# Kernel tuning notes

Measured on AMD Instinct MI355X. Metric: run time of the kernel, lower is better.

The kernel has to match this reference:

```python
import jax, jax.numpy as jnp
import numpy as np

A = 32          # num input capsule types
PSIZE = 16      # caps_size (pose matrix 4x4)
MD = 4          # mat_dim = sqrt(caps_size)
NCLS = 10       # output capsules / classes
KF = 5          # routing kernel (final_shape)
KK = KF * KF
KKA = KK * A
ITERS = 3
FINAL_LAMBDA = 0.01
EPS = 1e-12
LN2PI = float(np.log(2.0 * np.pi))
BN_EPS = 1e-5


def unfold(x, k, stride, pad):
    # torch.nn.functional.unfold: [b,C,h,w] -> [b, C*k*k, L], (c, kh, kw) channel-major
    b, c, h, w = x.shape
    if pad:
        x = jnp.pad(x, ((0, 0), (0, 0), (pad, pad), (pad, pad)))
    oh = (h + 2 * pad - k) // stride + 1
    ow = (w + 2 * pad - k) // stride + 1
    cols = jnp.stack([
        jnp.stack([x[:, :, i:i + stride * oh:stride, j:j + stride * ow:stride]
                   for j in range(k)], axis=3)
        for i in range(k)], axis=2)          # [b, c, k, k, oh, ow]
    return cols.reshape(b, c * k * k, oh * ow)


def conv3x3(x, w):
    return jax.lax.conv_general_dilated(x, w, (1, 1), [(1, 1), (1, 1)],
                                        dimension_numbers=('NCHW', 'OIHW', 'NCHW'))


def bn_inf(x, g, b, m, v):
    scale = g / jnp.sqrt(v + BN_EPS)
    return (x - m[None, :, None, None]) * scale[None, :, None, None] + b[None, :, None, None]


def em_routing(a_in, pose, W, beta_u, beta_a):
    b = a_in.shape[0]
    # pose votes
    pu = unfold(pose, KF, 1, 0)                     # [b, A*PSIZE*KK, l]
    l = pu.shape[-1]
    pu = pu.reshape(b, A, PSIZE, KK, l).transpose(0, 4, 3, 1, 2).reshape(b, l, KKA, PSIZE)
    pm = pu.reshape(b, l, KKA, MD, MD)[:, :, :, None]        # [b,l,kkA,1,md,md]
    v = jnp.matmul(pm, W)                                    # [b,l,kkA,B,md,md]
    v = v.reshape(b, l, KKA, NCLS, PSIZE)
    # activations
    au = unfold(a_in, KF, 1, 0).reshape(b, A, KK, l).transpose(0, 3, 2, 1).reshape(b, l, KKA)
    r = jnp.ones((b, l, KKA, NCLS, 1), v.dtype)
    a_out = mu = None
    for i in range(ITERS):
        lam = FINAL_LAMBDA * (1.0 - 0.95 ** (i + 1))
        # M-step
        rw = r * au[:, :, :, None, None]
        r_sum = rw.sum(axis=2, keepdims=True)                # [b,l,1,B,1]
        coeff = rw / (r_sum + EPS)
        mu = (coeff * v).sum(axis=2, keepdims=True)          # [b,l,1,B,psize]
        sigma_sq = (coeff * (v - mu) ** 2).sum(axis=2, keepdims=True) + EPS
        r_s = r_sum[:, :, 0]                                 # [b,l,B,1]
        sig = sigma_sq[:, :, 0]                              # [b,l,B,psize]
        cost_h = (beta_u + 0.5 * jnp.log(sig)) * r_s         # log(sqrt(s)) = 0.5*log(s)
        a_out = jax.nn.sigmoid(lam * (beta_a - cost_h.sum(axis=3)))   # [b,l,B]
        if i < ITERS - 1:
            # E-step (note: log(sigma_sq * ln2pi) as in original code)
            ln_p = (-0.5 * jnp.sum(jnp.log(sigma_sq * LN2PI), axis=-1)
                    - jnp.sum((v - mu) ** 2 / (2.0 * sigma_sq), axis=-1))   # [b,l,kkA,B]
            ln_ap = ln_p + jnp.log(a_out)[:, :, None, :]
            r = jax.nn.softmax(ln_ap, axis=-1)[..., None]
    oh = int(np.floor(np.sqrt(l)))
    pose_out = mu[:, :, 0].reshape(b, l, -1).transpose(0, 2, 1).reshape(b, -1, oh, oh)
    a_map = a_out.transpose(0, 2, 1).reshape(b, -1, oh, oh)
    return a_map, pose_out


def setup_inputs():
    key = jax.random.key(0)
    ks = jax.random.split(key, 14)
    batch = 256
    x = jax.random.normal(ks[0], (batch, 512, 5, 5), jnp.float32)
    w_a = jax.random.normal(ks[1], (A, 512, 3, 3), jnp.float32) * 0.02
    w_pose = jax.random.normal(ks[2], (A * PSIZE, 512, 3, 3), jnp.float32) * 0.02
    bn_a_g = 1.0 + 0.1 * jax.random.normal(ks[3], (A,), jnp.float32)
    bn_a_b = 0.1 * jax.random.normal(ks[4], (A,), jnp.float32)
    bn_a_m = 0.1 * jax.random.normal(ks[5], (A,), jnp.float32)
    bn_a_v = jax.random.uniform(ks[6], (A,), jnp.float32, 0.5, 1.5)
    C2 = A * PSIZE
    bn_p_g = 1.0 + 0.1 * jax.random.normal(ks[7], (C2,), jnp.float32)
    bn_p_b = 0.1 * jax.random.normal(ks[8], (C2,), jnp.float32)
    bn_p_m = 0.1 * jax.random.normal(ks[9], (C2,), jnp.float32)
    bn_p_v = jax.random.uniform(ks[10], (C2,), jnp.float32, 0.5, 1.5)
    W = jax.random.normal(ks[11], (KKA, NCLS, MD, MD), jnp.float32) * 0.25
    beta_u = jnp.zeros((1, 1, NCLS, 1), jnp.float32)
    beta_a = jnp.zeros((1, 1, NCLS), jnp.float32)
    return {"x": x, "w_a": w_a, "w_pose": w_pose,
            "bn_a_g": bn_a_g, "bn_a_b": bn_a_b, "bn_a_m": bn_a_m, "bn_a_v": bn_a_v,
            "bn_p_g": bn_p_g, "bn_p_b": bn_p_b, "bn_p_m": bn_p_m, "bn_p_v": bn_p_v,
            "W": W, "beta_u": beta_u, "beta_a": beta_a}


def reference(x, w_a, w_pose, bn_a_g, bn_a_b, bn_a_m, bn_a_v,
              bn_p_g, bn_p_b, bn_p_m, bn_p_v, W, beta_u, beta_a):
    a = jax.nn.sigmoid(bn_inf(conv3x3(x, w_a), bn_a_g, bn_a_b, bn_a_m, bn_a_v))
    pose = bn_inf(conv3x3(x, w_pose), bn_p_g, bn_p_b, bn_p_m, bn_p_v)
    a_map, _ = em_routing(a, pose, W, beta_u, beta_a)
    out = a_map.reshape(a_map.shape[0], -1)          # [b, 10]
    out = out / out.sum(axis=1, keepdims=True)
    return jnp.log(out)
```

## Files before the change

kernel.cpp:

```cpp
#include <hip/hip_runtime.h>
#include <math.h>

#define CIN 512
#define NCLS 10
#define KDIM 4608
#define NTOT 6400
#define MPAD 640
#define BK 128
#define NKT 36
#define NABLK (5 * NKT)
#define LN2PI_F 1.8378770664093453f

typedef __attribute__((ext_vector_type(8))) short bf16x8;
typedef __attribute__((ext_vector_type(4))) float f32x4;

typedef const __attribute__((address_space(1))) void* gas_ptr;
typedef __attribute__((address_space(3))) void* las_ptr;

__device__ __forceinline__ void async_copy16(const void* g, void* l) {
    __builtin_amdgcn_global_load_lds((gas_ptr)g, (las_ptr)l, 16, 0, 0);
}

__device__ __forceinline__ unsigned short f2bf(float f) {
    unsigned int u = __float_as_uint(f);
    u = (u + 0x7fffu + ((u >> 16) & 1u)) >> 16;
    return (unsigned short)u;
}
__device__ __forceinline__ float bf2f(unsigned short s) {
    return __uint_as_float(((unsigned int)s) << 16);
}
__device__ __forceinline__ float fexp(float x) { return __expf(x); }
__device__ __forceinline__ float flog(float x) { return __logf(x); }

__global__ __launch_bounds__(256) void pack_a_kernel(
    const float* __restrict__ w_pose, const float* __restrict__ w_a,
    const float* __restrict__ bn_p_g, const float* __restrict__ bn_p_b,
    const float* __restrict__ bn_p_m, const float* __restrict__ bn_p_v,
    const float* __restrict__ bn_a_g, const float* __restrict__ bn_a_b,
    const float* __restrict__ bn_a_m, const float* __restrict__ bn_a_v,
    const float* __restrict__ Wm,
    unsigned short* __restrict__ At, unsigned short* __restrict__ Wmb,
    float* __restrict__ sc, float* __restrict__ bi)
{
    const int blk = blockIdx.x;
    const int t = threadIdx.x;

    if (blk >= NABLK) {
        const int chunk = (blk - NABLK) * 256 + t;
        if (chunk < 16000) {
            const int e = chunk >> 1, half = chunk & 1;
            const int m = e / 10, c = e - m * 10;
            const int kk = m >> 5, a = m & 31;
            const int de = (kk * 10 + c) * 32 + a;
            const float4* s4 = reinterpret_cast<const float4*>(Wm + (size_t)chunk * 8);
            float4 x0 = s4[0], x1 = s4[1];
            int4 o;
            o.x = (int)f2bf(x0.x) | ((int)f2bf(x0.y) << 16);
            o.y = (int)f2bf(x0.z) | ((int)f2bf(x0.w) << 16);
            o.z = (int)f2bf(x1.x) | ((int)f2bf(x1.y) << 16);
            o.w = (int)f2bf(x1.z) | ((int)f2bf(x1.w) << 16);
            reinterpret_cast<int4*>(Wmb + ((size_t)de * 2 + half) * 8)[0] = o;
        }
        return;
    }

    const int mblk = blk / NKT;
    if (blk == 0) {
        for (int i = t; i < MPAD; i += 256) {
            float s = 0.f, b = 0.f;
            if (i < 512) {
                s = bn_p_g[i] / sqrtf(bn_p_v[i] + 1e-5f);
                b = bn_p_b[i] - bn_p_m[i] * s;
            } else if (i < 544) {
                const int j = i - 512;
                s = bn_a_g[j] / sqrtf(bn_a_v[j] + 1e-5f);
                b = bn_a_b[j] - bn_a_m[j] * s;
            }
            sc[i] = s; bi[i] = b;
        }
    }

    const int kt = blk - mblk * NKT;
    #pragma unroll
    for (int j = 0; j < 8; ++j) {
        const int c = t + j * 256;
        const int kc8 = c >> 7, slot = c & 127;
        const int row = mblk * 128 + (slot ^ (kc8 << 2));
        const int k0 = (kt * 16 + kc8) * 8;
        float v[8] = {0.f,0.f,0.f,0.f,0.f,0.f,0.f,0.f};
        if (row < 512) {
            const float4* s4 = reinterpret_cast<const float4*>(w_pose + (size_t)row * KDIM + k0);
            float4 x0 = s4[0], x1 = s4[1];
            v[0]=x0.x; v[1]=x0.y; v[2]=x0.z; v[3]=x0.w;
            v[4]=x1.x; v[5]=x1.y; v[6]=x1.z; v[7]=x1.w;
        } else if (row < 544) {
            const float4* s4 = reinterpret_cast<const float4*>(w_a + (size_t)(row - 512) * KDIM + k0);
            float4 x0 = s4[0], x1 = s4[1];
            v[0]=x0.x; v[1]=x0.y; v[2]=x0.z; v[3]=x0.w;
            v[4]=x1.x; v[5]=x1.y; v[6]=x1.z; v[7]=x1.w;
        }
        int4 o;
        o.x = (int)f2bf(v[0]) | ((int)f2bf(v[1]) << 16);
        o.y = (int)f2bf(v[2]) | ((int)f2bf(v[3]) << 16);
        o.z = (int)f2bf(v[4]) | ((int)f2bf(v[5]) << 16);
        o.w = (int)f2bf(v[6]) | ((int)f2bf(v[7]) << 16);
        reinterpret_cast<int4*>(At + ((((size_t)blk) << 11) + c) * 8)[0] = o;
    }
}

__global__ __launch_bounds__(1024) void pack_b_kernel(
    const float* __restrict__ x, unsigned short* __restrict__ Bt)
{
    __shared__ __align__(16) float xs[CIN * 25];
    const int b = blockIdx.x;
    const int t = threadIdx.x;
    const float4* xb = reinterpret_cast<const float4*>(x + (size_t)b * (CIN * 25));
    for (int f4 = t; f4 < (CIN * 25) / 4; f4 += 1024)
        reinterpret_cast<float4*>(xs)[f4] = xb[f4];
    __syncthreads();

    for (int w = t; w < 25 * (KDIM / 8); w += 1024) {
        const int ch = w / 25;
        const int px = w - ch * 25;
        const int py = px / 5, qx = px % 5;
        const int k0 = ch * 8;
        unsigned short v[8];
        #pragma unroll
        for (int j = 0; j < 8; ++j) {
            const int k = k0 + j;
            const int ci = k / 9;
            const int kk = k - ci * 9;
            const int dy = kk / 3, dx = kk - dy * 3;
            const int yy = py + dy - 1, xx = qx + dx - 1;
            const bool ok = (yy >= 0) & (yy < 5) & (xx >= 0) & (xx < 5);
            v[j] = ok ? f2bf(xs[ci * 25 + yy * 5 + xx]) : (unsigned short)0;
        }
        int4 o;
        o.x = (int)v[0] | ((int)v[1] << 16);
        o.y = (int)v[2] | ((int)v[3] << 16);
        o.z = (int)v[4] | ((int)v[5] << 16);
        o.w = (int)v[6] | ((int)v[7] << 16);
        const int n = b * 25 + px;
        const int nblk = n >> 7, nr = n & 127;
        const int kt = k0 >> 7;
        const int kc8 = (k0 >> 3) & 15;
        const int c = kc8 * 128 + (nr ^ (kc8 << 2));
        reinterpret_cast<int4*>(Bt + ((((size_t)(nblk * NKT + kt)) << 11) + c) * 8)[0] = o;
    }
}

__global__ __launch_bounds__(1024) void gemm_kernel(
    const unsigned short* __restrict__ At,
    const unsigned short* __restrict__ Bt,
    const float* __restrict__ sc, const float* __restrict__ bi,
    unsigned short* __restrict__ Cp,
    float* __restrict__ Ca)
{
    __shared__ __align__(16) unsigned char smem[131072];
    const int t = threadIdx.x;
    const int L = blockIdx.x;
    int mblk, nblk;
    if (L >= 240) { const int i = L - 240; mblk = i >> 1; nblk = 48 + (i & 1); }
    else          { const int q = L / 40, r = L - q * 40;
                    mblk = r >> 3; nblk = q * 8 + (r & 7); }
    const int m0 = mblk * 128, n0 = nblk * 128;
    const int lane = t & 63, w = t >> 6;
    const int g = w >> 2, wq = w & 3;
    const int wm = wq >> 1, wn = wq & 1;
    const int row16 = lane & 15, quad = lane >> 4;

    f32x4 acc[4][4] = {};

    const unsigned short* gAbase = At + (((size_t)mblk * NKT) << 14);
    const unsigned short* gBbase = Bt + (((size_t)nblk * NKT) << 14);

    #define STAGE(kt, s)                                                      \
    {                                                                         \
        unsigned short* As_ = (unsigned short*)(smem + (s) * 65536);          \
        unsigned short* Bs_ = As_ + 16384;                                    \
        const unsigned short* ga = gAbase + ((size_t)(kt) << 14);             \
        const unsigned short* gb = gBbase + ((size_t)(kt) << 14);             \
        _Pragma("unroll")                                                     \
        for (int j = 0; j < 2; ++j) {                                         \
            async_copy16(ga + ((size_t)(j * 1024 + t) << 3),                  \
                         As_ + ((size_t)(j * 1024 + w * 64) << 3));           \
            async_copy16(gb + ((size_t)(j * 1024 + t) << 3),                  \
                         Bs_ + ((size_t)(j * 1024 + w * 64) << 3));           \
        }                                                                     \
    }

    #define COMPUTE(s)                                                        \
    {                                                                         \
        const unsigned short* As_ = (const unsigned short*)(smem + (s) * 65536);\
        const unsigned short* Bs_ = As_ + 16384;                              \
        const int kc8b = g * 4 + quad;                                        \
        const int sw = kc8b << 2;                                             \
        bf16x8 af[4], bfr[4];                                                 \
        _Pragma("unroll")                                                     \
        for (int mt = 0; mt < 4; ++mt)                                        \
            af[mt] = *reinterpret_cast<const bf16x8*>(                        \
                &As_[(size_t)(kc8b * 128 + ((wm * 64 + mt * 16 + row16) ^ sw)) * 8]);\
        _Pragma("unroll")                                                     \
        for (int nt = 0; nt < 4; ++nt)                                        \
            bfr[nt] = *reinterpret_cast<const bf16x8*>(                       \
                &Bs_[(size_t)(kc8b * 128 + ((wn * 64 + nt * 16 + row16) ^ sw)) * 8]);\
        _Pragma("unroll")                                                     \
        for (int mt = 0; mt < 4; ++mt)                                        \
            _Pragma("unroll")                                                 \
            for (int nt = 0; nt < 4; ++nt)                                    \
                acc[mt][nt] = __builtin_amdgcn_mfma_f32_16x16x32_bf16(        \
                    af[mt], bfr[nt], acc[mt][nt], 0, 0, 0);                   \
    }

    STAGE(0, 0);
    for (int kt = 0; kt < NKT; ++kt) {
        __syncthreads();
        if (kt + 1 < NKT) STAGE(kt + 1, (kt + 1) & 1);
        COMPUTE(kt & 1);
    }
    #undef STAGE
    #undef COMPUTE

    f32x4* mb = (f32x4*)smem;
    #pragma unroll
    for (int r = 1; r < 4; ++r) {
        __syncthreads();
        if (g == r) {
            f32x4* dst = mb + wq * 1024;
            #pragma unroll
            for (int i = 0; i < 16; ++i)
                dst[i * 64 + lane] = acc[i >> 2][i & 3];
        }
        __syncthreads();
        if (g == 0) {
            const f32x4* src = mb + wq * 1024;
            #pragma unroll
            for (int i = 0; i < 16; ++i)
                acc[i >> 2][i & 3] += src[i * 64 + lane];
        }
    }

    if (g == 0) {
        #pragma unroll
        for (int mt = 0; mt < 4; ++mt) {
            const int mbase = m0 + wm * 64 + mt * 16 + quad * 4;
            if (mbase >= 544) continue;
            #pragma unroll
            for (int rg = 0; rg < 4; ++rg) {
                const int m = mbase + rg;
                const float s = sc[m], bbx = bi[m];
                #pragma unroll
                for (int nt = 0; nt < 4; ++nt) {
                    const int n = n0 + wn * 64 + nt * 16 + row16;
                    const float v = fmaf(acc[mt][nt][rg], s, bbx);
                    if (m < 512) Cp[(size_t)m * NTOT + n] = f2bf(v);
                    else Ca[(size_t)(m - 512) * NTOT + n] = 1.f / (1.f + fexp(-v));
                }
            }
        }
    }
}

__global__ __launch_bounds__(640, 1) void em_kernel(
    const unsigned short* __restrict__ Cp,
    const float* __restrict__ Ca,
    const unsigned short* __restrict__ Wmb,
    const float* __restrict__ beta_u, const float* __restrict__ beta_a,
    float* __restrict__ out)
{
    __shared__ __align__(16) unsigned short psh[25][2][32][8];
    __shared__ float aush[800];
    __shared__ float lnq[NCLS][800];
    __shared__ float mu_sh[NCLS][16];
    __shared__ float i2s_sh[NCLS][16];
    __shared__ float costp[2][NCLS];
    __shared__ float slgp[2][NCLS];
    __shared__ float Kc_sh[NCLS];
    __shared__ float aout_sh[NCLS];

    const int b = blockIdx.x, t = threadIdx.x;
    const int c = t >> 6;
    const int rh = (t >> 5) & 1;
    const int a = t & 31;

    const unsigned short* pb = Cp + (size_t)b * 25;
    for (int f = t; f < 12800; f += 640) {
        const int c2 = f / 25, px = f - c2 * 25;
        const int e = c2 & 15;
        psh[px][e >> 3][c2 >> 4][e & 7] = pb[(size_t)c2 * NTOT + px];
    }
    const float* ab = Ca + (size_t)b * 25;
    for (int f = t; f < 800; f += 640) {
        const int ci = f / 25, px = f - ci * 25;
        aush[px * 32 + ci] = ab[(size_t)ci * NTOT + px];
    }
    __syncthreads();

    const float bu = beta_u[c], ba = beta_a[c];
    float muL[8], i2sL[8], KcL = 0.f;
    const unsigned short* wbase = Wmb + ((size_t)(c * 32 + a)) * 16;

    #define VOTE(w0_, w1_, p_, vv)                                           \
        {                                                                    \
            float pm[8], wv[16];                                             \
            const unsigned int pu[4] = {(unsigned)p_.x, (unsigned)p_.y,      \
                                        (unsigned)p_.z, (unsigned)p_.w};     \
            _Pragma("unroll")                                                \
            for (int i = 0; i < 4; ++i) {                                    \
                pm[2*i]   = __uint_as_float(pu[i] << 16);                    \
                pm[2*i+1] = __uint_as_float(pu[i] & 0xFFFF0000u);            \
            }                                                                \
            const unsigned int uu[8] = {(unsigned)w0_.x,(unsigned)w0_.y,     \
                (unsigned)w0_.z,(unsigned)w0_.w,(unsigned)w1_.x,             \
                (unsigned)w1_.y,(unsigned)w1_.z,(unsigned)w1_.w};            \
            _Pragma("unroll")                                                \
            for (int i = 0; i < 8; ++i) {                                    \
                wv[2*i]   = __uint_as_float(uu[i] << 16);                    \
                wv[2*i+1] = __uint_as_float(uu[i] & 0xFFFF0000u);            \
            }                                                                \
            _Pragma("unroll")                                                \
            for (int jr = 0; jr < 2; ++jr) {                                 \
                _Pragma("unroll")                                            \
                for (int s = 0; s < 4; ++s) {                                \
                    float av = 0.f;                                          \
                    _Pragma("unroll")                                        \
                    for (int tt = 0; tt < 4; ++tt)                           \
                        av = fmaf(pm[jr*4+tt], wv[tt*4+s], av);              \
                    vv[jr*4+s] = av;                                         \
                }                                                            \
            }                                                                \
        }

    float p95 = 1.f;
    for (int it = 0; it < 3; ++it) {
        p95 *= 0.95f;
        const float lam = 0.01f * (1.f - p95);

        if (it > 0) {
            int4 wr0 = *reinterpret_cast<const int4*>(wbase);
            int4 wr1 = *reinterpret_cast<const int4*>(wbase + 8);
            int4 pr  = *reinterpret_cast<const int4*>(&psh[0][rh][a][0]);
            for (int kk = 0; kk < 25; ++kk) {
                const int4 w0 = wr0, w1 = wr1, p = pr;
                if (kk < 24) {
                    const unsigned short* wn = wbase + (size_t)(kk + 1) * 5120;
                    wr0 = *reinterpret_cast<const int4*>(wn);
                    wr1 = *reinterpret_cast<const int4*>(wn + 8);
                    pr  = *reinterpret_cast<const int4*>(&psh[kk + 1][rh][a][0]);
                }
                float vv[8];
                VOTE(w0, w1, p, vv);
                float q = (rh == 0) ? KcL : 0.f;
                #pragma unroll
                for (int j = 0; j < 8; ++j) {
                    const float d = vv[j] - muL[j];
                    q -= d * d * i2sL[j];
                }
                q += __shfl_xor(q, 32);
                if (rh == 0) lnq[c][kk * 32 + a] = q;
            }
            __syncthreads();
            for (int m = t; m < 800; m += 640) {
                float qv[NCLS];
                #pragma unroll
                for (int cc = 0; cc < NCLS; ++cc) qv[cc] = lnq[cc][m];
                float mx = qv[0];
                #pragma unroll
                for (int cc = 1; cc < NCLS; ++cc) mx = fmaxf(mx, qv[cc]);
                float ev[NCLS];
                float den = 0.f;
                #pragma unroll
                for (int cc = 0; cc < NCLS; ++cc) {
                    ev[cc] = fexp(qv[cc] - mx);
                    den += ev[cc];
                }
                const float s = aush[m] * __builtin_amdgcn_rcpf(den);
                #pragma unroll
                for (int cc = 0; cc < NCLS; ++cc)
                    lnq[cc][m] = ev[cc] * s;
            }
            __syncthreads();
        }

        float S0 = 0.f, S1[8], S2[8];
        #pragma unroll
        for (int j = 0; j < 8; ++j) { S1[j] = 0.f; S2[j] = 0.f; }

        int4 wA0 = *reinterpret_cast<const int4*>(wbase);
        int4 wA1 = *reinterpret_cast<const int4*>(wbase + 8);
        int4 wB0 = *reinterpret_cast<const int4*>(wbase + 5120);
        int4 wB1 = *reinterpret_cast<const int4*>(wbase + 5120 + 8);
        int4 pr  = *reinterpret_cast<const int4*>(&psh[0][rh][a][0]);
        for (int kk = 0; kk < 25; ++kk) {
            const int4 w0 = wA0, w1 = wA1, p = pr;
            wA0 = wB0; wA1 = wB1;
            if (kk < 23) {
                const unsigned short* wn = wbase + (size_t)(kk + 2) * 5120;
                wB0 = *reinterpret_cast<const int4*>(wn);
                wB1 = *reinterpret_cast<const int4*>(wn + 8);
            }
            if (kk < 24)
                pr = *reinterpret_cast<const int4*>(&psh[kk + 1][rh][a][0]);
            float vv[8];
            VOTE(w0, w1, p, vv);
            const int m = kk * 32 + a;
            const float rw = (it == 0) ? aush[m] : lnq[c][m];
            S0 += rw;
            #pragma unroll
            for (int j = 0; j < 8; ++j) {
                const float rv = rw * vv[j];
                S1[j] += rv;
                S2[j] = fmaf(rv, vv[j], S2[j]);
            }
        }

        #pragma unroll
        for (int off = 16; off >= 1; off >>= 1) {
            S0 += __shfl_xor(S0, off);
            #pragma unroll
            for (int j = 0; j < 8; ++j) {
                S1[j] += __shfl_xor(S1[j], off);
                S2[j] += __shfl_xor(S2[j], off);
            }
        }

        if (a == 0) {
            const float s0e = S0 + 1e-12f;
            const float inv = 1.f / s0e;
            float cost_ = 0.f, slg_ = 0.f;
            #pragma unroll
            for (int j = 0; j < 8; ++j) {
                const float mu_ = S1[j] * inv;
                const float sg = (S2[j] - 2.f * mu_ * S1[j] + mu_ * mu_ * S0) * inv
                                 + 1e-12f;
                cost_ += bu + 0.5f * flog(sg);
                slg_ += flog(sg * LN2PI_F);
                mu_sh[c][rh * 8 + j] = mu_;
                i2s_sh[c][rh * 8 + j] = 0.5f / sg;
            }
            costp[rh][c] = cost_;
            slgp[rh][c] = slg_;
        }
        __syncthreads();
        if (a == 0 && rh == 0) {
            const float costsum = (costp[0][c] + costp[1][c]) * S0;
            const float aout = 1.f / (1.f + fexp(-(lam * (ba - costsum))));
            aout_sh[c] = aout;
            Kc_sh[c] = flog(aout) - 0.5f * (slgp[0][c] + slgp[1][c]);
        }
        __syncthreads();
        if (it < 2) {
            #pragma unroll
            for (int j = 0; j < 8; ++j) {
                muL[j] = mu_sh[c][rh * 8 + j];
                i2sL[j] = i2s_sh[c][rh * 8 + j];
            }
            KcL = Kc_sh[c];
        }
    }

    if (t < NCLS) {
        float s = 0.f;
        #pragma unroll
        for (int cc = 0; cc < NCLS; ++cc) s += aout_sh[cc];
        out[b * NCLS + t] = flog(aout_sh[t] / s);
    }
    #undef VOTE
}

extern "C" void kernel_launch(void* const* d_in, const int* in_sizes, int n_in,
                              void* d_out, int out_size, void* d_ws, size_t ws_size,
                              hipStream_t stream) {
    const float* x      = (const float*)d_in[0];
    const float* w_a    = (const float*)d_in[1];
    const float* w_pose = (const float*)d_in[2];
    const float* bn_a_g = (const float*)d_in[3];
    const float* bn_a_b = (const float*)d_in[4];
    const float* bn_a_m = (const float*)d_in[5];
    const float* bn_a_v = (const float*)d_in[6];
    const float* bn_p_g = (const float*)d_in[7];
    const float* bn_p_b = (const float*)d_in[8];
    const float* bn_p_m = (const float*)d_in[9];
    const float* bn_p_v = (const float*)d_in[10];
    const float* Wm     = (const float*)d_in[11];
    const float* beta_u = (const float*)d_in[12];
    const float* beta_a = (const float*)d_in[13];
    float* out = (float*)d_out;

    char* p = (char*)d_ws;
    unsigned short* At  = (unsigned short*)p;  p += (size_t)MPAD * KDIM * 2;
    unsigned short* Bt  = (unsigned short*)p;  p += (size_t)NTOT * KDIM * 2;
    unsigned short* Wmb = (unsigned short*)p;  p += (size_t)800 * NCLS * 16 * 2;
    unsigned short* Cp  = (unsigned short*)p;  p += (size_t)512 * NTOT * 2;
    float* Ca = (float*)p;                     p += (size_t)32 * NTOT * 4;
    float* sc = (float*)p;                     p += MPAD * 4;
    float* bi = (float*)p;                     p += MPAD * 4;

    pack_a_kernel<<<NABLK + 63, 256, 0, stream>>>(w_pose, w_a,
                                                  bn_p_g, bn_p_b, bn_p_m, bn_p_v,
                                                  bn_a_g, bn_a_b, bn_a_m, bn_a_v,
                                                  Wm, At, Wmb, sc, bi);
    pack_b_kernel<<<256, 1024, 0, stream>>>(x, Bt);
    gemm_kernel<<<250, 1024, 0, stream>>>(At, Bt, sc, bi, Cp, Ca);
    em_kernel<<<256, 640, 0, stream>>>(Cp, Ca, Wmb, beta_u, beta_a, out);
}
```

Measured before the change: 227.0 us.

## Merge pack kernels and stage EM routing weights through LDS with async copies

Combines the A/W packing kernel and the im2col B packing kernel into one launch, removing a kernel boundary. In the EM kernel, the per-thread global loads of the transformation matrices are replaced by double-buffered async global-to-LDS copies in chunks of four kernel positions, read back with a swizzled index. This aims to cut launch overhead and make weight loads coalesced and overlapped with compute. In exchange it adds about 80KB of LDS and a block barrier per chunk in every routing pass, and the merged pack kernel's 1024-thread blocks reserve 51KB of LDS even where it is unused.

```diff
diff --git a/kernel.cpp b/kernel.cpp
--- a/kernel.cpp
+++ b/kernel.cpp
@@ -32,7 +32,8 @@
 __device__ __forceinline__ float fexp(float x) { return __expf(x); }
 __device__ __forceinline__ float flog(float x) { return __logf(x); }
 
-__global__ __launch_bounds__(256) void pack_a_kernel(
+__global__ __launch_bounds__(1024) void pack_kernel(
+    const float* __restrict__ x,
     const float* __restrict__ w_pose, const float* __restrict__ w_a,
     const float* __restrict__ bn_p_g, const float* __restrict__ bn_p_b,
     const float* __restrict__ bn_p_m, const float* __restrict__ bn_p_v,
@@ -40,13 +41,57 @@
     const float* __restrict__ bn_a_m, const float* __restrict__ bn_a_v,
     const float* __restrict__ Wm,
     unsigned short* __restrict__ At, unsigned short* __restrict__ Wmb,
-    float* __restrict__ sc, float* __restrict__ bi)
+    float* __restrict__ sc, float* __restrict__ bi,
+    unsigned short* __restrict__ Bt)
 {
-    const int blk = blockIdx.x;
+    __shared__ __align__(16) float xs[CIN * 25];
+    const int bid = blockIdx.x;
     const int t = threadIdx.x;
 
-    if (blk >= NABLK) {
-        const int chunk = (blk - NABLK) * 256 + t;
+    if (bid < 256) {
+        const int b = bid;
+        const float4* xb = reinterpret_cast<const float4*>(x + (size_t)b * (CIN * 25));
+        for (int f4 = t; f4 < (CIN * 25) / 4; f4 += 1024)
+            reinterpret_cast<float4*>(xs)[f4] = xb[f4];
+        __syncthreads();
+
+        for (int w = t; w < 25 * (KDIM / 8); w += 1024) {
+            const int ch = w / 25;
+            const int px = w - ch * 25;
+            const int py = px / 5, qx = px % 5;
+            const int k0 = ch * 8;
+            unsigned short v[8];
+            #pragma unroll
+            for (int j = 0; j < 8; ++j) {
+                const int k = k0 + j;
+                const int ci = k / 9;
+                const int kk = k - ci * 9;
+                const int dy = kk / 3, dx = kk - dy * 3;
+                const int yy = py + dy - 1, xx = qx + dx - 1;
+                const bool ok = (yy >= 0) & (yy < 5) & (xx >= 0) & (xx < 5);
+                v[j] = ok ? f2bf(xs[ci * 25 + yy * 5 + xx]) : (unsigned short)0;
+            }
+            int4 o;
+            o.x = (int)v[0] | ((int)v[1] << 16);
+            o.y = (int)v[2] | ((int)v[3] << 16);
+            o.z = (int)v[4] | ((int)v[5] << 16);
+            o.w = (int)v[6] | ((int)v[7] << 16);
+            const int n = b * 25 + px;
+            const int nblk = n >> 7, nr = n & 127;
+            const int kt = k0 >> 7;
+            const int kc8 = (k0 >> 3) & 15;
+            const int c = kc8 * 128 + (nr ^ (kc8 << 2));
+            reinterpret_cast<int4*>(Bt + ((((size_t)(nblk * NKT + kt)) << 11) + c) * 8)[0] = o;
+        }
+        return;
+    }
+
+    const int f = (bid - 256) * 1024 + t;
+    const int vblk = f >> 8, vt = f & 255;
+    if (vblk >= NABLK + 63) return;
+
+    if (vblk >= NABLK) {
+        const int chunk = (vblk - NABLK) * 256 + vt;
         if (chunk < 16000) {
             const int e = chunk >> 1, half = chunk & 1;
             const int m = e / 10, c = e - m * 10;
@@ -64,9 +109,9 @@
         return;
     }
 
-    const int mblk = blk / NKT;
-    if (blk == 0) {
-        for (int i = t; i < MPAD; i += 256) {
+    const int mblk = vblk / NKT;
+    if (vblk == 0) {
+        for (int i = vt; i < MPAD; i += 256) {
             float s = 0.f, b = 0.f;
             if (i < 512) {
                 s = bn_p_g[i] / sqrtf(bn_p_v[i] + 1e-5f);
@@ -80,10 +125,10 @@
         }
     }
 
-    const int kt = blk - mblk * NKT;
+    const int kt = vblk - mblk * NKT;
     #pragma unroll
     for (int j = 0; j < 8; ++j) {
-        const int c = t + j * 256;
+        const int c = vt + j * 256;
         const int kc8 = c >> 7, slot = c & 127;
         const int row = mblk * 128 + (slot ^ (kc8 << 2));
         const int k0 = (kt * 16 + kc8) * 8;
@@ -104,48 +149,7 @@
         o.y = (int)f2bf(v[2]) | ((int)f2bf(v[3]) << 16);
         o.z = (int)f2bf(v[4]) | ((int)f2bf(v[5]) << 16);
         o.w = (int)f2bf(v[6]) | ((int)f2bf(v[7]) << 16);
-        reinterpret_cast<int4*>(At + ((((size_t)blk) << 11) + c) * 8)[0] = o;
-    }
-}
-
-__global__ __launch_bounds__(1024) void pack_b_kernel(
-    const float* __restrict__ x, unsigned short* __restrict__ Bt)
-{
-    __shared__ __align__(16) float xs[CIN * 25];
-    const int b = blockIdx.x;
-    const int t = threadIdx.x;
-    const float4* xb = reinterpret_cast<const float4*>(x + (size_t)b * (CIN * 25));
-    for (int f4 = t; f4 < (CIN * 25) / 4; f4 += 1024)
-        reinterpret_cast<float4*>(xs)[f4] = xb[f4];
-    __syncthreads();
-
-    for (int w = t; w < 25 * (KDIM / 8); w += 1024) {
-        const int ch = w / 25;
-        const int px = w - ch * 25;
-        const int py = px / 5, qx = px % 5;
-        const int k0 = ch * 8;
-        unsigned short v[8];
-        #pragma unroll
-        for (int j = 0; j < 8; ++j) {
-            const int k = k0 + j;
-            const int ci = k / 9;
-            const int kk = k - ci * 9;
-            const int dy = kk / 3, dx = kk - dy * 3;
-            const int yy = py + dy - 1, xx = qx + dx - 1;
-            const bool ok = (yy >= 0) & (yy < 5) & (xx >= 0) & (xx < 5);
-            v[j] = ok ? f2bf(xs[ci * 25 + yy * 5 + xx]) : (unsigned short)0;
-        }
-        int4 o;
-        o.x = (int)v[0] | ((int)v[1] << 16);
-        o.y = (int)v[2] | ((int)v[3] << 16);
-        o.z = (int)v[4] | ((int)v[5] << 16);
-        o.w = (int)v[6] | ((int)v[7] << 16);
-        const int n = b * 25 + px;
-        const int nblk = n >> 7, nr = n & 127;
-        const int kt = k0 >> 7;
-        const int kc8 = (k0 >> 3) & 15;
-        const int c = kc8 * 128 + (nr ^ (kc8 << 2));
-        reinterpret_cast<int4*>(Bt + ((((size_t)(nblk * NKT + kt)) << 11) + c) * 8)[0] = o;
+        reinterpret_cast<int4*>(At + ((((size_t)vblk) << 11) + c) * 8)[0] = o;
     }
 }
 
@@ -269,6 +273,7 @@
     float* __restrict__ out)
 {
     __shared__ __align__(16) unsigned short psh[25][2][32][8];
+    __shared__ __align__(16) unsigned short wsh[2 * 20480];
     __shared__ float aush[800];
     __shared__ float lnq[NCLS][800];
     __shared__ float mu_sh[NCLS][16];
@@ -283,6 +288,20 @@
     const int rh = (t >> 5) & 1;
     const int a = t & 31;
 
+    const int gu = t ^ ((t >> 3) & 3);
+    const int r2 = (c * 32 + a) * 2;
+    const int u0 = r2 ^ ((r2 >> 3) & 3);
+
+    #define STAGEW(qq, ss)                                                   \
+    {                                                                        \
+        const int nkk_ = ((qq) == 6) ? 1 : 4;                                \
+        const unsigned short* gW = Wmb + (size_t)(qq) * 4 * 5120;            \
+        unsigned short* lW = wsh + (size_t)(ss) * 20480;                     \
+        for (int kki = 0; kki < nkk_; ++kki)                                 \
+            async_copy16(gW + (size_t)(kki * 640 + gu) * 8,                  \
+                         lW + (size_t)(kki * 640 + t) * 8);                  \
+    }
+
     const unsigned short* pb = Cp + (size_t)b * 25;
     for (int f = t; f < 12800; f += 640) {
         const int c2 = f / 25, px = f - c2 * 25;
@@ -298,7 +317,6 @@
 
     const float bu = beta_u[c], ba = beta_a[c];
     float muL[8], i2sL[8], KcL = 0.f;
-    const unsigned short* wbase = Wmb + ((size_t)(c * 32 + a)) * 16;
 
     #define VOTE(w0_, w1_, p_, vv)                                           \
         {                                                                    \
@@ -337,29 +355,33 @@
         const float lam = 0.01f * (1.f - p95);
 
         if (it > 0) {
-            int4 wr0 = *reinterpret_cast<const int4*>(wbase);
-            int4 wr1 = *reinterpret_cast<const int4*>(wbase + 8);
-            int4 pr  = *reinterpret_cast<const int4*>(&psh[0][rh][a][0]);
-            for (int kk = 0; kk < 25; ++kk) {
-                const int4 w0 = wr0, w1 = wr1, p = pr;
-                if (kk < 24) {
-                    const unsigned short* wn = wbase + (size_t)(kk + 1) * 5120;
-                    wr0 = *reinterpret_cast<const int4*>(wn);
-                    wr1 = *reinterpret_cast<const int4*>(wn + 8);
-                    pr  = *reinterpret_cast<const int4*>(&psh[kk + 1][rh][a][0]);
+            STAGEW(0, 0);
+            __syncthreads();
+            for (int qc = 0; qc < 7; ++qc) {
+                if (qc < 6) STAGEW(qc + 1, (qc + 1) & 1);
+                const unsigned short* wb = wsh + (size_t)(qc & 1) * 20480;
+                #pragma unroll
+                for (int kkin = 0; kkin < 4; ++kkin) {
+                    const int kk = qc * 4 + kkin;
+                    if (kk < 25) {
+                        const unsigned short* wrow = wb + kkin * 5120;
+                        const int4 w0 = *reinterpret_cast<const int4*>(wrow + (size_t)u0 * 8);
+                        const int4 w1 = *reinterpret_cast<const int4*>(wrow + (size_t)(u0 ^ 1) * 8);
+                        const int4 p = *reinterpret_cast<const int4*>(&psh[kk][rh][a][0]);
+                        float vv[8];
+                        VOTE(w0, w1, p, vv);
+                        float qacc = (rh == 0) ? KcL : 0.f;
+                        #pragma unroll
+                        for (int j = 0; j < 8; ++j) {
+                            const float d = vv[j] - muL[j];
+                            qacc -= d * d * i2sL[j];
+                        }
+                        qacc += __shfl_xor(qacc, 32);
+                        if (rh == 0) lnq[c][kk * 32 + a] = qacc;
+                    }
                 }
-                float vv[8];
-                VOTE(w0, w1, p, vv);
-                float q = (rh == 0) ? KcL : 0.f;
-                #pragma unroll
-                for (int j = 0; j < 8; ++j) {
-                    const float d = vv[j] - muL[j];
-                    q -= d * d * i2sL[j];
-                }
-                q += __shfl_xor(q, 32);
-                if (rh == 0) lnq[c][kk * 32 + a] = q;
-            }
-            __syncthreads();
+                __syncthreads();
+            }
             for (int m = t; m < 800; m += 640) {
                 float qv[NCLS];
                 #pragma unroll
@@ -386,32 +408,33 @@
         #pragma unroll
         for (int j = 0; j < 8; ++j) { S1[j] = 0.f; S2[j] = 0.f; }
 
-        int4 wA0 = *reinterpret_cast<const int4*>(wbase);
-        int4 wA1 = *reinterpret_cast<const int4*>(wbase + 8);
-        int4 wB0 = *reinterpret_cast<const int4*>(wbase + 5120);
-        int4 wB1 = *reinterpret_cast<const int4*>(wbase + 5120 + 8);
-        int4 pr  = *reinterpret_cast<const int4*>(&psh[0][rh][a][0]);
-        for (int kk = 0; kk < 25; ++kk) {
-            const int4 w0 = wA0, w1 = wA1, p = pr;
-            wA0 = wB0; wA1 = wB1;
-            if (kk < 23) {
-                const unsigned short* wn = wbase + (size_t)(kk + 2) * 5120;
-                wB0 = *reinterpret_cast<const int4*>(wn);
-                wB1 = *reinterpret_cast<const int4*>(wn + 8);
-            }
-            if (kk < 24)
-                pr = *reinterpret_cast<const int4*>(&psh[kk + 1][rh][a][0]);
-            float vv[8];
-            VOTE(w0, w1, p, vv);
-            const int m = kk * 32 + a;
-            const float rw = (it == 0) ? aush[m] : lnq[c][m];
-            S0 += rw;
-            #pragma unroll
-            for (int j = 0; j < 8; ++j) {
-                const float rv = rw * vv[j];
-                S1[j] += rv;
-                S2[j] = fmaf(rv, vv[j], S2[j]);
-            }
+        STAGEW(0, 0);
+        __syncthreads();
+        for (int qc = 0; qc < 7; ++qc) {
+            if (qc < 6) STAGEW(qc + 1, (qc + 1) & 1);
+            const unsigned short* wb = wsh + (size_t)(qc & 1) * 20480;
+            #pragma unroll
+            for (int kkin = 0; kkin < 4; ++kkin) {
+                const int kk = qc * 4 + kkin;
+                if (kk < 25) {
+                    const unsigned short* wrow = wb + kkin * 5120;
+                    const int4 w0 = *reinterpret_cast<const int4*>(wrow + (size_t)u0 * 8);
+                    const int4 w1 = *reinterpret_cast<const int4*>(wrow + (size_t)(u0 ^ 1) * 8);
+                    const int4 p = *reinterpret_cast<const int4*>(&psh[kk][rh][a][0]);
+                    float vv[8];
+                    VOTE(w0, w1, p, vv);
+                    const int m = kk * 32 + a;
+                    const float rw = (it == 0) ? aush[m] : lnq[c][m];
+                    S0 += rw;
+                    #pragma unroll
+                    for (int j = 0; j < 8; ++j) {
+                        const float rv = rw * vv[j];
+                        S1[j] += rv;
+                        S2[j] = fmaf(rv, vv[j], S2[j]);
+                    }
+                }
+            }
+            __syncthreads();
         }
 
         #pragma unroll
@@ -466,6 +489,7 @@
         out[b * NCLS + t] = flog(aout_sh[t] / s);
     }
     #undef VOTE
+    #undef STAGEW
 }
 
 extern "C" void kernel_launch(void* const* d_in, const int* in_sizes, int n_in,
@@ -496,11 +520,10 @@
     float* sc = (float*)p;                     p += MPAD * 4;
     float* bi = (float*)p;                     p += MPAD * 4;
 
-    pack_a_kernel<<<NABLK + 63, 256, 0, stream>>>(w_pose, w_a,
-                                                  bn_p_g, bn_p_b, bn_p_m, bn_p_v,
-                                                  bn_a_g, bn_a_b, bn_a_m, bn_a_v,
-                                                  Wm, At, Wmb, sc, bi);
-    pack_b_kernel<<<256, 1024, 0, stream>>>(x, Bt);
+    pack_kernel<<<317, 1024, 0, stream>>>(x, w_pose, w_a,
+                                          bn_p_g, bn_p_b, bn_p_m, bn_p_v,
+                                          bn_a_g, bn_a_b, bn_a_m, bn_a_v,
+                                          Wm, At, Wmb, sc, bi, Bt);
     gemm_kernel<<<250, 1024, 0, stream>>>(At, Bt, sc, bi, Cp, Ca);
     em_kernel<<<256, 640, 0, stream>>>(Cp, Ca, Wmb, beta_u, beta_a, out);
 }
```

Result: no change. 230.9 us (+1.7%).

## Split EM routing per batch across two workgroups with flag-synchronized partial sums

Applied to the files above, without the earlier changes.

Each batch element's EM routing is now handled by two blocks, each processing about half of the 25 kernel positions, doubling the grid to 512 blocks. After each M-step reduction, the blocks publish their partial sums to global memory and exchange them via release/acquire flags before continuing. This aims to use more CUs and shorten the serial per-block loop. The cost is extra global traffic, spin-wait synchronization, and a reliance on paired blocks being co-resident to avoid deadlock.

```diff
diff --git a/kernel.cpp b/kernel.cpp
--- a/kernel.cpp
+++ b/kernel.cpp
@@ -40,7 +40,8 @@
     const float* __restrict__ bn_a_m, const float* __restrict__ bn_a_v,
     const float* __restrict__ Wm,
     unsigned short* __restrict__ At, unsigned short* __restrict__ Wmb,
-    float* __restrict__ sc, float* __restrict__ bi)
+    float* __restrict__ sc, float* __restrict__ bi,
+    int* __restrict__ flags)
 {
     const int blk = blockIdx.x;
     const int t = threadIdx.x;
@@ -78,6 +79,7 @@
             }
             sc[i] = s; bi[i] = b;
         }
+        for (int i = t; i < 512; i += 256) flags[i] = 0;
     }
 
     const int kt = blk - mblk * NKT;
@@ -266,11 +268,13 @@
     const float* __restrict__ Ca,
     const unsigned short* __restrict__ Wmb,
     const float* __restrict__ beta_u, const float* __restrict__ beta_a,
+    float* __restrict__ part,
+    int* __restrict__ flags,
     float* __restrict__ out)
 {
-    __shared__ __align__(16) unsigned short psh[25][2][32][8];
-    __shared__ float aush[800];
-    __shared__ float lnq[NCLS][800];
+    __shared__ __align__(16) unsigned short psh[13][2][32][8];
+    __shared__ float aush[416];
+    __shared__ float lnq[NCLS][416];
     __shared__ float mu_sh[NCLS][16];
     __shared__ float i2s_sh[NCLS][16];
     __shared__ float costp[2][NCLS];
@@ -278,27 +282,36 @@
     __shared__ float Kc_sh[NCLS];
     __shared__ float aout_sh[NCLS];
 
-    const int b = blockIdx.x, t = threadIdx.x;
+    const int bid = blockIdx.x;
+    const int b = bid >> 1, half = bid & 1;
+    const int t = threadIdx.x;
     const int c = t >> 6;
     const int rh = (t >> 5) & 1;
     const int a = t & 31;
-
-    const unsigned short* pb = Cp + (size_t)b * 25;
-    for (int f = t; f < 12800; f += 640) {
-        const int c2 = f / 25, px = f - c2 * 25;
+    const int klo = half ? 13 : 0;
+    const int knum = half ? 12 : 13;
+    const int NM = knum << 5;
+
+    int* myFlag  = flags + b * 2 + half;
+    int* othFlag = flags + b * 2 + (half ^ 1);
+
+    const unsigned short* pb = Cp + (size_t)b * 25 + klo;
+    for (int f = t; f < (knum << 9); f += 640) {
+        const int c2 = f / knum, pxl = f - c2 * knum;
         const int e = c2 & 15;
-        psh[px][e >> 3][c2 >> 4][e & 7] = pb[(size_t)c2 * NTOT + px];
-    }
-    const float* ab = Ca + (size_t)b * 25;
-    for (int f = t; f < 800; f += 640) {
-        const int ci = f / 25, px = f - ci * 25;
-        aush[px * 32 + ci] = ab[(size_t)ci * NTOT + px];
+        psh[pxl][e >> 3][c2 >> 4][e & 7] = pb[(size_t)c2 * NTOT + pxl];
+    }
+    const float* ab = Ca + (size_t)b * 25 + klo;
+    for (int f = t; f < NM; f += 640) {
+        const int pxl = f >> 5, ci = f & 31;
+        aush[pxl * 32 + ci] = ab[(size_t)ci * NTOT + pxl];
     }
     __syncthreads();
 
     const float bu = beta_u[c], ba = beta_a[c];
     float muL[8], i2sL[8], KcL = 0.f;
-    const unsigned short* wbase = Wmb + ((size_t)(c * 32 + a)) * 16;
+    const unsigned short* wlo = Wmb + ((size_t)(c * 32 + a)) * 16
+                                    + (size_t)klo * 5120;
 
     #define VOTE(w0_, w1_, p_, vv)                                           \
         {                                                                    \
@@ -337,13 +350,13 @@
         const float lam = 0.01f * (1.f - p95);
 
         if (it > 0) {
-            int4 wr0 = *reinterpret_cast<const int4*>(wbase);
-            int4 wr1 = *reinterpret_cast<const int4*>(wbase + 8);
+            int4 wr0 = *reinterpret_cast<const int4*>(wlo);
+            int4 wr1 = *reinterpret_cast<const int4*>(wlo + 8);
             int4 pr  = *reinterpret_cast<const int4*>(&psh[0][rh][a][0]);
-            for (int kk = 0; kk < 25; ++kk) {
+            for (int kk = 0; kk < knum; ++kk) {
                 const int4 w0 = wr0, w1 = wr1, p = pr;
-                if (kk < 24) {
-                    const unsigned short* wn = wbase + (size_t)(kk + 1) * 5120;
+                if (kk + 1 < knum) {
+                    const unsigned short* wn = wlo + (size_t)(kk + 1) * 5120;
                     wr0 = *reinterpret_cast<const int4*>(wn);
                     wr1 = *reinterpret_cast<const int4*>(wn + 8);
                     pr  = *reinterpret_cast<const int4*>(&psh[kk + 1][rh][a][0]);
@@ -360,7 +373,8 @@
                 if (rh == 0) lnq[c][kk * 32 + a] = q;
             }
             __syncthreads();
-            for (int m = t; m < 800; m += 640) {
+            if (t < NM) {
+                const int m = t;
                 float qv[NCLS];
                 #pragma unroll
                 for (int cc = 0; cc < NCLS; ++cc) qv[cc] = lnq[cc][m];
@@ -386,20 +400,20 @@
         #pragma unroll
         for (int j = 0; j < 8; ++j) { S1[j] = 0.f; S2[j] = 0.f; }
 
-        int4 wA0 = *reinterpret_cast<const int4*>(wbase);
-        int4 wA1 = *reinterpret_cast<const int4*>(wbase + 8);
-        int4 wB0 = *reinterpret_cast<const int4*>(wbase + 5120);
-        int4 wB1 = *reinterpret_cast<const int4*>(wbase + 5120 + 8);
+        int4 wA0 = *reinterpret_cast<const int4*>(wlo);
+        int4 wA1 = *reinterpret_cast<const int4*>(wlo + 8);
+        int4 wB0 = *reinterpret_cast<const int4*>(wlo + 5120);
+        int4 wB1 = *reinterpret_cast<const int4*>(wlo + 5120 + 8);
         int4 pr  = *reinterpret_cast<const int4*>(&psh[0][rh][a][0]);
-        for (int kk = 0; kk < 25; ++kk) {
+        for (int kk = 0; kk < knum; ++kk) {
             const int4 w0 = wA0, w1 = wA1, p = pr;
             wA0 = wB0; wA1 = wB1;
-            if (kk < 23) {
-                const unsigned short* wn = wbase + (size_t)(kk + 2) * 5120;
+            if (kk + 2 < knum) {
+                const unsigned short* wn = wlo + (size_t)(kk + 2) * 5120;
                 wB0 = *reinterpret_cast<const int4*>(wn);
                 wB1 = *reinterpret_cast<const int4*>(wn + 8);
             }
-            if (kk < 24)
+            if (kk + 1 < knum)
                 pr = *reinterpret_cast<const int4*>(&psh[kk + 1][rh][a][0]);
             float vv[8];
             VOTE(w0, w1, p, vv);
@@ -421,6 +435,54 @@
             for (int j = 0; j < 8; ++j) {
                 S1[j] += __shfl_xor(S1[j], off);
                 S2[j] += __shfl_xor(S2[j], off);
+            }
+        }
+
+        float* myPart = part + ((size_t)((b * 2 + half) * 3 + it)) * (NCLS * 33);
+        const float* othPart =
+            part + ((size_t)((b * 2 + (half ^ 1)) * 3 + it)) * (NCLS * 33);
+        if (a == 0) {
+            const int base = c * 33;
+            if (rh == 0) {
+                __hip_atomic_store(&myPart[base], S0,
+                                   __ATOMIC_RELAXED, __HIP_MEMORY_SCOPE_AGENT);
+                #pragma unroll
+                for (int j = 0; j < 8; ++j) {
+                    __hip_atomic_store(&myPart[base + 1 + j], S1[j],
+                                       __ATOMIC_RELAXED, __HIP_MEMORY_SCOPE_AGENT);
+                    __hip_atomic_store(&myPart[base + 9 + j], S2[j],
+                                       __ATOMIC_RELAXED, __HIP_MEMORY_SCOPE_AGENT);
+                }
+            } else {
+                #pragma unroll
+                for (int j = 0; j < 8; ++j) {
+                    __hip_atomic_store(&myPart[base + 17 + j], S1[j],
+                                       __ATOMIC_RELAXED, __HIP_MEMORY_SCOPE_AGENT);
+                    __hip_atomic_store(&myPart[base + 25 + j], S2[j],
+                                       __ATOMIC_RELAXED, __HIP_MEMORY_SCOPE_AGENT);
+                }
+            }
+        }
+        __syncthreads();
+        if (t == 0) {
+            __hip_atomic_store(myFlag, it + 1,
+                               __ATOMIC_RELEASE, __HIP_MEMORY_SCOPE_AGENT);
+            while (__hip_atomic_load(othFlag, __ATOMIC_ACQUIRE,
+                                     __HIP_MEMORY_SCOPE_AGENT) < it + 1)
+                __builtin_amdgcn_s_sleep(2);
+        }
+        __syncthreads();
+        if (a == 0) {
+            const int base = c * 33;
+            S0 += __hip_atomic_load(&othPart[base],
+                                    __ATOMIC_RELAXED, __HIP_MEMORY_SCOPE_AGENT);
+            const int o1 = rh ? 17 : 1, o2 = rh ? 25 : 9;
+            #pragma unroll
+            for (int j = 0; j < 8; ++j) {
+                S1[j] += __hip_atomic_load(&othPart[base + o1 + j],
+                                           __ATOMIC_RELAXED, __HIP_MEMORY_SCOPE_AGENT);
+                S2[j] += __hip_atomic_load(&othPart[base + o2 + j],
+                                           __ATOMIC_RELAXED, __HIP_MEMORY_SCOPE_AGENT);
             }
         }
 
@@ -459,7 +521,7 @@
         }
     }
 
-    if (t < NCLS) {
+    if (half == 0 && t < NCLS) {
         float s = 0.f;
         #pragma unroll
         for (int cc = 0; cc < NCLS; ++cc) s += aout_sh[cc];
@@ -495,12 +557,15 @@
     float* Ca = (float*)p;                     p += (size_t)32 * NTOT * 4;
     float* sc = (float*)p;                     p += MPAD * 4;
     float* bi = (float*)p;                     p += MPAD * 4;
+    float* part = (float*)p;                   p += (size_t)256 * 2 * 3 * NCLS * 33 * 4;
+    int* flags = (int*)p;                      p += (size_t)512 * 4;
 
     pack_a_kernel<<<NABLK + 63, 256, 0, stream>>>(w_pose, w_a,
                                                   bn_p_g, bn_p_b, bn_p_m, bn_p_v,
                                                   bn_a_g, bn_a_b, bn_a_m, bn_a_v,
-                                                  Wm, At, Wmb, sc, bi);
+                                                  Wm, At, Wmb, sc, bi, flags);
     pack_b_kernel<<<256, 1024, 0, stream>>>(x, Bt);
     gemm_kernel<<<250, 1024, 0, stream>>>(At, Bt, sc, bi, Cp, Ca);
-    em_kernel<<<256, 640, 0, stream>>>(Cp, Ca, Wmb, beta_u, beta_a, out);
-}
+    em_kernel<<<512, 640, 0, stream>>>(Cp, Ca, Wmb, beta_u, beta_a,
+                                       part, flags, out);
+}
```

Result: slower. 284.9 us (+25.5%).
